# Kernel tuning notes

Measured on AMD Instinct MI355X. Metric: run time of the kernel, lower is better.

## Reference

```python
import jax, jax.numpy as jnp
import numpy as np

N, IN_DIM, H, K = 4096, 64, 64, 3
DT = 0.05


def graph_filter(z, S_powers, W):
    # z: [N, d_in], S_powers: [K, N, N], W: [K, d_in, d_out]
    zk = jnp.einsum('knm,md->knd', S_powers, z)   # K-hop diffused features
    return jnp.einsum('knd,kde->ne', zk, W)       # sum over taps k


def setup_inputs() -> dict:
    key = jax.random.key(0)
    ks = jax.random.split(key, 8)
    w_scale = 0.1
    return {
        'x': jax.random.normal(ks[0], (N, H), jnp.float32),
        'u': jax.random.normal(ks[1], (N, IN_DIM), jnp.float32),
        'S_powers': jax.random.normal(ks[2], (K, N, N), jnp.float32) / np.float32(np.sqrt(N)),
        'WA_hat': jax.random.normal(ks[3], (K, H, H), jnp.float32) * w_scale,
        'WB_hat': jax.random.normal(ks[4], (K, IN_DIM, H), jnp.float32) * w_scale,
        'WA_state': jax.random.normal(ks[5], (K, H, H), jnp.float32) * w_scale,
        'WB_state': jax.random.normal(ks[6], (K, IN_DIM, H), jnp.float32) * w_scale,
        'bx': jnp.zeros((1, H), jnp.float32),
        'bu': jnp.zeros((1, H), jnp.float32),
        'b': jnp.ones((1, H), jnp.float32) * 0.1,
        'n_steps': 4,
    }


def reference(x, u, S_powers, WA_hat, WB_hat, WA_state, WB_state, bx, bu, b, n_steps):
    # Input-driven terms are constant across solver steps; hoist them.
    fu = jax.nn.relu(graph_filter(u, S_powers, WB_hat) + bu)   # [N, H]
    sigma_c = jnp.tanh(graph_filter(u, S_powers, WB_state))    # [N, H]

    def step(xc, _):
        f = jax.nn.relu(graph_filter(xc, S_powers, WA_hat) + bx) + fu
        dx = -(b + f) * xc - graph_filter(xc, S_powers, WA_state) + f * sigma_c
        xn = jnp.clip(xc + DT * dx, -1.0, 1.0)
        return xn, None

    xf, _ = jax.lax.scan(step, x, None, length=n_steps)
    return xf
```

## Files before the change

### kernel.cpp

```cpp
#include <hip/hip_runtime.h>
#include <math.h>


typedef unsigned short u16;
typedef unsigned int u32;
typedef __attribute__((ext_vector_type(8))) short short8;
typedef __attribute__((ext_vector_type(4))) float f32x4;

#define NN 4096
#define HD 64
#define KB32 128
#define DT_C 0.05f

__device__ __forceinline__ u16 f2bf(float f) {
    u32 u = __float_as_uint(f);
    u += 0x7FFFu + ((u >> 16) & 1u);
    return (u16)(u >> 16);
}
__device__ __forceinline__ u32 pk2(float a, float b) {
    return (u32)f2bf(a) | ((u32)f2bf(b) << 16);
}

__global__ __launch_bounds__(256) void zprep_kernel(
    const float* __restrict__ u, const float* __restrict__ x,
    const float* __restrict__ WAh, const float* __restrict__ WAs,
    const float* __restrict__ WBh, const float* __restrict__ WBs,
    u16* __restrict__ utT, u16* __restrict__ xtT, u16* __restrict__ WtT)
{
    const int b = blockIdx.x;
    const int t = threadIdx.x;
    if (b < 256) {
        const float* z = (b < 128) ? u : x;
        u16* ztT = (b < 128) ? utT : xtT;
        const int kb = b & 127, n0 = kb * 32;
        __shared__ __align__(16) u16 tile[64][40];
        const int nl = t >> 3, c0 = (t & 7) * 8;
        const float* src = z + (size_t)(n0 + nl) * HD + c0;
        float4 f0 = ((const float4*)src)[0];
        float4 f1 = ((const float4*)src)[1];
        tile[c0 + 0][nl] = f2bf(f0.x); tile[c0 + 1][nl] = f2bf(f0.y);
        tile[c0 + 2][nl] = f2bf(f0.z); tile[c0 + 3][nl] = f2bf(f0.w);
        tile[c0 + 4][nl] = f2bf(f1.x); tile[c0 + 5][nl] = f2bf(f1.y);
        tile[c0 + 6][nl] = f2bf(f1.z); tile[c0 + 7][nl] = f2bf(f1.w);
        __syncthreads();
        const int e = t >> 2, kw0 = (t & 3) * 8;
        short8 v = *(const short8*)&tile[e][kw0];
        *(short8*)(ztT + ((size_t)kb * 64 + e) * 32 + kw0) = v;
    } else {
        for (int f = t; f < 4 * 6 * 64 * 32; f += 256) {
            int mat = f / 12288, r = f % 12288;
            int s = r / 2048, r2 = r % 2048;
            int e = r2 >> 5, kw = r2 & 31;
            int kp = s * 32 + kw, tap = kp >> 6, d = kp & 63;
            const float* Wm = (mat == 0) ? WAh : (mat == 1) ? WAs : (mat == 2) ? WBh : WBs;
            WtT[f] = f2bf(Wm[((size_t)tap * HD + d) * HD + e]);
        }
    }
}

__global__ __launch_bounds__(256) void diffuseA_kernel(
    const float* __restrict__ S, const u16* __restrict__ utT,
    const u16* __restrict__ xtT, u16* __restrict__ SbT,
    float* __restrict__ Yp, int iters)
{
    const int t = threadIdx.x;
    const int tap = blockIdx.z;
    const int row0 = blockIdx.x * 64;
    const int kb0 = blockIdx.y * iters;
    const int w = t >> 6, lane = t & 63, l15 = lane & 15, quad = lane >> 4;

    const int r0 = row0 + w * 16 + l15;
    const float* Sb = S + ((size_t)tap * NN + r0) * NN + quad * 8;
    u16* Wb = SbT + (((size_t)tap * KB32) * NN + r0) * 32 + quad * 8;

    f32x4 z4 = {0.f, 0.f, 0.f, 0.f};
    f32x4 acc[2][4];
    #pragma unroll
    for (int s = 0; s < 2; ++s)
        #pragma unroll
        for (int j = 0; j < 4; ++j) acc[s][j] = z4;

    #pragma unroll 4
    for (int it = 0; it < iters; ++it) {
        const int kb = kb0 + it;
        const float* sp0 = Sb + (size_t)kb * 32;
        float4 f0 = ((const float4*)sp0)[0];
        float4 f1 = ((const float4*)sp0)[1];
        union U { uint4 u4; short8 s8; };
        U A0;
        A0.u4.x = pk2(f0.x, f0.y); A0.u4.y = pk2(f0.z, f0.w);
        A0.u4.z = pk2(f1.x, f1.y); A0.u4.w = pk2(f1.z, f1.w);
        *(uint4*)(Wb + (size_t)kb * (NN * 32)) = A0.u4;
        #pragma unroll
        for (int ct = 0; ct < 4; ++ct) {
            const size_t bo = ((size_t)kb * 64 + ct * 16 + l15) * 32 + quad * 8;
            short8 bu = *(const short8*)(utT + bo);
            short8 bx = *(const short8*)(xtT + bo);
            acc[0][ct] = __builtin_amdgcn_mfma_f32_16x16x32_bf16(A0.s8, bu, acc[0][ct], 0, 0, 0);
            acc[1][ct] = __builtin_amdgcn_mfma_f32_16x16x32_bf16(A0.s8, bx, acc[1][ct], 0, 0, 0);
        }
    }
    #pragma unroll
    for (int s = 0; s < 2; ++s) {
        float* yb = Yp + ((size_t)((blockIdx.y * 3 + tap) * 2 + s) * NN + row0) * HD;
        #pragma unroll
        for (int ct = 0; ct < 4; ++ct)
            #pragma unroll
            for (int r = 0; r < 4; ++r)
                yb[(size_t)(w * 16 + quad * 4 + r) * HD + ct * 16 + l15] = acc[s][ct][r];
    }
}

__global__ __launch_bounds__(256) void diffuseS_kernel(
    const u16* __restrict__ SbT, const u16* __restrict__ xtT,
    float* __restrict__ Yp, int iters)
{
    const int t = threadIdx.x;
    const int tap = blockIdx.z;
    const int row0 = blockIdx.x * 64;
    const int kb0 = blockIdx.y * iters;
    const int w = t >> 6, lane = t & 63, l15 = lane & 15, quad = lane >> 4;

    const u16* A0 = SbT + (((size_t)(tap * KB32) * NN + row0 + w * 16 + l15) * 32) + quad * 8;
    const size_t arowstride = (size_t)NN * 32;

    f32x4 z4 = {0.f, 0.f, 0.f, 0.f};
    f32x4 acc[4];
    #pragma unroll
    for (int j = 0; j < 4; ++j) acc[j] = z4;

    #pragma unroll 4
    for (int it = 0; it < iters; ++it) {
        const int kb = kb0 + it;
        short8 a0 = *(const short8*)(A0 + (size_t)kb * arowstride);
        #pragma unroll
        for (int ct = 0; ct < 4; ++ct) {
            short8 bb = *(const short8*)(xtT + ((size_t)kb * 64 + ct * 16 + l15) * 32 + quad * 8);
            acc[ct] = __builtin_amdgcn_mfma_f32_16x16x32_bf16(a0, bb, acc[ct], 0, 0, 0);
        }
    }
    float* yb = Yp + ((size_t)(blockIdx.y * 3 + tap) * NN + row0) * HD;
    #pragma unroll
    for (int ct = 0; ct < 4; ++ct)
        #pragma unroll
        for (int r = 0; r < 4; ++r)
            yb[(size_t)(w * 16 + quad * 4 + r) * HD + ct * 16 + l15] = acc[ct][r];
}

__global__ __launch_bounds__(256) void update_step_kernel(
    const float* __restrict__ Yp, int KS, const u16* __restrict__ WtT,
    const float* __restrict__ bx, const float* __restrict__ bvec,
    const float* __restrict__ fu, const float* __restrict__ sc,
    const float* __restrict__ xc, float* __restrict__ xn,
    u16* __restrict__ xtT, int do_pack)
{
    __shared__ __align__(16) u16 yt[6][16][56];
    __shared__ __align__(16) u16 pkt[64][24];
    const int t = threadIdx.x;
    const int n0 = blockIdx.x * 16;

    for (int f = t; f < 384; f += 256) {
        const int tap = f >> 7;
        const int r = f & 127;
        const int nl = r >> 3, d8 = r & 7, d0 = d8 * 8;
        const float* p = Yp + ((size_t)tap * NN + n0 + nl) * HD + d0;
        const size_t kstride = (size_t)3 * NN * HD;
        float4 s0 = {0.f, 0.f, 0.f, 0.f}, s1 = {0.f, 0.f, 0.f, 0.f};
        for (int y = 0; y < KS; ++y) {
            float4 v0 = ((const float4*)(p + (size_t)y * kstride))[0];
            float4 v1 = ((const float4*)(p + (size_t)y * kstride))[1];
            s0.x += v0.x; s0.y += v0.y; s0.z += v0.z; s0.w += v0.w;
            s1.x += v1.x; s1.y += v1.y; s1.z += v1.z; s1.w += v1.w;
        }
        uint4 o;
        o.x = pk2(s0.x, s0.y); o.y = pk2(s0.z, s0.w);
        o.z = pk2(s1.x, s1.y); o.w = pk2(s1.z, s1.w);
        const int s = tap * 2 + (d8 >> 2), kw0 = (d8 & 3) * 8;
        *(uint4*)&yt[s][nl][kw0] = o;
    }
    __syncthreads();

    const int wv = t >> 6, lane = t & 63, l15 = lane & 15, quad = lane >> 4;
    f32x4 z4 = {0.f, 0.f, 0.f, 0.f};
    f32x4 aF = z4, aG = z4;
    #pragma unroll
    for (int s = 0; s < 6; ++s) {
        short8 a = *(const short8*)&yt[s][l15][quad * 8];
        const size_t wo = ((size_t)s * 64 + wv * 16 + l15) * 32 + quad * 8;
        short8 bF = *(const short8*)(WtT + wo);
        short8 bG = *(const short8*)(WtT + wo + 12288);
        aF = __builtin_amdgcn_mfma_f32_16x16x32_bf16(a, bF, aF, 0, 0, 0);
        aG = __builtin_amdgcn_mfma_f32_16x16x32_bf16(a, bG, aG, 0, 0, 0);
    }
    const int e = wv * 16 + l15;
    const float bxv = bx[e], bbv = bvec[e];
    float xos[4];
    #pragma unroll
    for (int r = 0; r < 4; ++r) {
        const int n = n0 + quad * 4 + r;
        const size_t o = (size_t)n * HD + e;
        float ff = fmaxf(aF[r] + bxv, 0.f) + fu[o];
        float xv = xc[o];
        float dx = -(bbv + ff) * xv - aG[r] + ff * sc[o];
        float xo = fminf(fmaxf(xv + DT_C * dx, -1.f), 1.f);
        xn[o] = xo;
        xos[r] = xo;
    }
    if (do_pack) {
        uint2 pv;
        pv.x = pk2(xos[0], xos[1]);
        pv.y = pk2(xos[2], xos[3]);
        *(uint2*)&pkt[e][quad * 4] = pv;
        __syncthreads();
        if (t < 128) {
            const int ee = t >> 1, g = t & 1;
            short8 v = *(const short8*)&pkt[ee][g * 8];
            const int kb = n0 >> 5;
            const int kwb = (n0 & 31) + g * 8;
            *(short8*)(xtT + ((size_t)kb * 64 + ee) * 32 + kwb) = v;
        }
    }
}

__global__ __launch_bounds__(256) void update1_kernel(
    const float* __restrict__ Yp, int KS, const u16* __restrict__ WtT,
    const float* __restrict__ bx, const float* __restrict__ bu,
    const float* __restrict__ bvec, const float* __restrict__ x0,
    float* __restrict__ fu, float* __restrict__ sc, float* __restrict__ x1,
    u16* __restrict__ xtT)
{
    __shared__ __align__(16) u16 yt[2][6][16][56];
    __shared__ __align__(16) u16 pkt[64][24];
    const int t = threadIdx.x;
    const int n0 = blockIdx.x * 16;

    #pragma unroll
    for (int ff = 0; ff < 3; ++ff) {
        const int f = t + ff * 256;
        const int src = f / 384;
        const int r3 = f - src * 384;
        const int tap = r3 >> 7;
        const int r = r3 & 127;
        const int nl = r >> 3, d8 = r & 7, d0 = d8 * 8;
        const float* p = Yp + (((size_t)(tap * 2 + src)) * NN + n0 + nl) * HD + d0;
        const size_t kstride = (size_t)6 * NN * HD;
        float4 s0 = {0.f, 0.f, 0.f, 0.f}, s1 = {0.f, 0.f, 0.f, 0.f};
        for (int y = 0; y < KS; ++y) {
            float4 v0 = ((const float4*)(p + (size_t)y * kstride))[0];
            float4 v1 = ((const float4*)(p + (size_t)y * kstride))[1];
            s0.x += v0.x; s0.y += v0.y; s0.z += v0.z; s0.w += v0.w;
            s1.x += v1.x; s1.y += v1.y; s1.z += v1.z; s1.w += v1.w;
        }
        uint4 o;
        o.x = pk2(s0.x, s0.y); o.y = pk2(s0.z, s0.w);
        o.z = pk2(s1.x, s1.y); o.w = pk2(s1.z, s1.w);
        const int s = tap * 2 + (d8 >> 2), kw0 = (d8 & 3) * 8;
        *(uint4*)&yt[src][s][nl][kw0] = o;
    }
    __syncthreads();

    const int wv = t >> 6, lane = t & 63, l15 = lane & 15, quad = lane >> 4;
    f32x4 z4 = {0.f, 0.f, 0.f, 0.f};
    f32x4 aF = z4, aG = z4, aFu = z4, aSc = z4;
    #pragma unroll
    for (int s = 0; s < 6; ++s) {
        short8 au = *(const short8*)&yt[0][s][l15][quad * 8];
        short8 ax = *(const short8*)&yt[1][s][l15][quad * 8];
        const size_t wo = ((size_t)s * 64 + wv * 16 + l15) * 32 + quad * 8;
        short8 bF  = *(const short8*)(WtT + wo);
        short8 bG  = *(const short8*)(WtT + wo + 12288);
        short8 bFu = *(const short8*)(WtT + wo + 2 * 12288);
        short8 bSc = *(const short8*)(WtT + wo + 3 * 12288);
        aF  = __builtin_amdgcn_mfma_f32_16x16x32_bf16(ax, bF,  aF,  0, 0, 0);
        aG  = __builtin_amdgcn_mfma_f32_16x16x32_bf16(ax, bG,  aG,  0, 0, 0);
        aFu = __builtin_amdgcn_mfma_f32_16x16x32_bf16(au, bFu, aFu, 0, 0, 0);
        aSc = __builtin_amdgcn_mfma_f32_16x16x32_bf16(au, bSc, aSc, 0, 0, 0);
    }
    const int e = wv * 16 + l15;
    const float bxv = bx[e], buv = bu[e], bbv = bvec[e];
    float xos[4];
    #pragma unroll
    for (int r = 0; r < 4; ++r) {
        const int n = n0 + quad * 4 + r;
        const size_t o = (size_t)n * HD + e;
        float fuv = fmaxf(aFu[r] + buv, 0.f);
        float scv = tanhf(aSc[r]);
        float ff = fmaxf(aF[r] + bxv, 0.f) + fuv;
        float xv = x0[o];
        float dx = -(bbv + ff) * xv - aG[r] + ff * scv;
        float xo = fminf(fmaxf(xv + DT_C * dx, -1.f), 1.f);
        fu[o] = fuv; sc[o] = scv; x1[o] = xo;
        xos[r] = xo;
    }
    {
        uint2 pv;
        pv.x = pk2(xos[0], xos[1]);
        pv.y = pk2(xos[2], xos[3]);
        *(uint2*)&pkt[e][quad * 4] = pv;
        __syncthreads();
        if (t < 128) {
            const int ee = t >> 1, g = t & 1;
            short8 v = *(const short8*)&pkt[ee][g * 8];
            const int kb = n0 >> 5;
            const int kwb = (n0 & 31) + g * 8;
            *(short8*)(xtT + ((size_t)kb * 64 + ee) * 32 + kwb) = v;
        }
    }
}

extern "C" void kernel_launch(void* const* d_in, const int* in_sizes, int n_in,
                              void* d_out, int out_size, void* d_ws, size_t ws_size,
                              hipStream_t stream) {
    const float* x   = (const float*)d_in[0];
    const float* u   = (const float*)d_in[1];
    const float* S   = (const float*)d_in[2];
    const float* WAh = (const float*)d_in[3];
    const float* WBh = (const float*)d_in[4];
    const float* WAs = (const float*)d_in[5];
    const float* WBs = (const float*)d_in[6];
    const float* bx  = (const float*)d_in[7];
    const float* bu  = (const float*)d_in[8];
    const float* bvec= (const float*)d_in[9];
    float* out = (float*)d_out;

    const size_t sbf_bytes = (size_t)3 * NN * NN * 2;
    const size_t slice = (size_t)NN * HD * 4;
    const size_t rest = 2 * 524288 + 98304 + 4 * 1048576;
    int KS_A = 8, KS_S = 8;
    if (ws_size < sbf_bytes + 48 * slice + rest) { KS_A = 4; KS_S = 8; }
    if (ws_size < sbf_bytes + 24 * slice + rest) { KS_A = 2; KS_S = 4; }
    if (ws_size < sbf_bytes + 12 * slice + rest) { KS_A = 1; KS_S = 2; }
    const int nslice = (KS_A * 6 > KS_S * 3) ? KS_A * 6 : KS_S * 3;

    char* p = (char*)d_ws;
    u16* SbT  = (u16*)p;         p += sbf_bytes;
    float* Yp = (float*)p;       p += (size_t)nslice * slice;
    u16* utT  = (u16*)p;         p += 524288;
    u16* xtT  = (u16*)p;         p += 524288;
    u16* WtT  = (u16*)p;         p += 98304;
    float* fu = (float*)p;       p += 1048576;
    float* sc = (float*)p;       p += 1048576;
    float* xA = (float*)p;       p += 1048576;
    float* xB = (float*)p;       p += 1048576;

    zprep_kernel<<<257, 256, 0, stream>>>(u, x, WAh, WAs, WBh, WBs, utT, xtT, WtT);

    diffuseA_kernel<<<dim3(64, KS_A, 3), 256, 0, stream>>>(S, utT, xtT, SbT, Yp, KB32 / KS_A);
    update1_kernel<<<256, 256, 0, stream>>>(Yp, KS_A, WtT, bx, bu, bvec, x, fu, sc, xA, xtT);

    diffuseS_kernel<<<dim3(64, KS_S, 3), 256, 0, stream>>>(SbT, xtT, Yp, KB32 / KS_S);
    update_step_kernel<<<256, 256, 0, stream>>>(Yp, KS_S, WtT, bx, bvec, fu, sc, xA, xB, xtT, 1);

    diffuseS_kernel<<<dim3(64, KS_S, 3), 256, 0, stream>>>(SbT, xtT, Yp, KB32 / KS_S);
    update_step_kernel<<<256, 256, 0, stream>>>(Yp, KS_S, WtT, bx, bvec, fu, sc, xB, xA, xtT, 1);

    diffuseS_kernel<<<dim3(64, KS_S, 3), 256, 0, stream>>>(SbT, xtT, Yp, KB32 / KS_S);
    update_step_kernel<<<256, 256, 0, stream>>>(Yp, KS_S, WtT, bx, bvec, fu, sc, xA, out, xtT, 0);
}
```

Before: 521.5 us.

## Fuse three taps per diffuseS block, swap MFMA operands for vector stores

diffuseS now handles all three taps in one block, so each loaded B fragment of xtT is reused across the three S taps instead of being reloaded per tap. The split-K factor for the step kernels rises from 8 to 16 to keep the grid filled after the tap dimension is removed. MFMA operand order is swapped in both diffuse kernels so each lane's accumulator holds contiguous output columns, allowing f32x4 vector stores in place of scalar strided stores. B loads in diffuseA are hoisted ahead of the conversion, and unroll drops from 4 to 2. The costs are more accumulator registers per thread and more partial-sum slices that the update kernel must reduce.

```diff
diff --git a/kernel.cpp b/kernel.cpp
--- a/kernel.cpp
+++ b/kernel.cpp
@@ -69,9 +69,9 @@
     const int kb0 = blockIdx.y * iters;
     const int w = t >> 6, lane = t & 63, l15 = lane & 15, quad = lane >> 4;
 
-    const int r0 = row0 + w * 16 + l15;
-    const float* Sb = S + ((size_t)tap * NN + r0) * NN + quad * 8;
-    u16* Wb = SbT + (((size_t)tap * KB32) * NN + r0) * 32 + quad * 8;
+    const int n = row0 + w * 16 + l15;
+    const float* Sb = S + ((size_t)tap * NN + n) * NN + quad * 8;
+    u16* Wb = SbT + (((size_t)tap * KB32) * NN + n) * 32 + quad * 8;
 
     f32x4 z4 = {0.f, 0.f, 0.f, 0.f};
     f32x4 acc[2][4];
@@ -80,12 +80,19 @@
         #pragma unroll
         for (int j = 0; j < 4; ++j) acc[s][j] = z4;
 
-    #pragma unroll 4
+    #pragma unroll 2
     for (int it = 0; it < iters; ++it) {
         const int kb = kb0 + it;
         const float* sp0 = Sb + (size_t)kb * 32;
         float4 f0 = ((const float4*)sp0)[0];
         float4 f1 = ((const float4*)sp0)[1];
+        short8 bu[4], bx[4];
+        #pragma unroll
+        for (int ct = 0; ct < 4; ++ct) {
+            const size_t bo = ((size_t)kb * 64 + ct * 16 + l15) * 32 + quad * 8;
+            bu[ct] = *(const short8*)(utT + bo);
+            bx[ct] = *(const short8*)(xtT + bo);
+        }
         union U { uint4 u4; short8 s8; };
         U A0;
         A0.u4.x = pk2(f0.x, f0.y); A0.u4.y = pk2(f0.z, f0.w);
@@ -93,21 +100,16 @@
         *(uint4*)(Wb + (size_t)kb * (NN * 32)) = A0.u4;
         #pragma unroll
         for (int ct = 0; ct < 4; ++ct) {
-            const size_t bo = ((size_t)kb * 64 + ct * 16 + l15) * 32 + quad * 8;
-            short8 bu = *(const short8*)(utT + bo);
-            short8 bx = *(const short8*)(xtT + bo);
-            acc[0][ct] = __builtin_amdgcn_mfma_f32_16x16x32_bf16(A0.s8, bu, acc[0][ct], 0, 0, 0);
-            acc[1][ct] = __builtin_amdgcn_mfma_f32_16x16x32_bf16(A0.s8, bx, acc[1][ct], 0, 0, 0);
+            acc[0][ct] = __builtin_amdgcn_mfma_f32_16x16x32_bf16(bu[ct], A0.s8, acc[0][ct], 0, 0, 0);
+            acc[1][ct] = __builtin_amdgcn_mfma_f32_16x16x32_bf16(bx[ct], A0.s8, acc[1][ct], 0, 0, 0);
         }
     }
     #pragma unroll
     for (int s = 0; s < 2; ++s) {
-        float* yb = Yp + ((size_t)((blockIdx.y * 3 + tap) * 2 + s) * NN + row0) * HD;
+        float* yb = Yp + ((size_t)((blockIdx.y * 3 + tap) * 2 + s) * NN + n) * HD + quad * 4;
         #pragma unroll
         for (int ct = 0; ct < 4; ++ct)
-            #pragma unroll
-            for (int r = 0; r < 4; ++r)
-                yb[(size_t)(w * 16 + quad * 4 + r) * HD + ct * 16 + l15] = acc[s][ct][r];
+            *(f32x4*)(yb + ct * 16) = acc[s][ct];
     }
 }
 
@@ -116,35 +118,46 @@
     float* __restrict__ Yp, int iters)
 {
     const int t = threadIdx.x;
-    const int tap = blockIdx.z;
     const int row0 = blockIdx.x * 64;
     const int kb0 = blockIdx.y * iters;
     const int w = t >> 6, lane = t & 63, l15 = lane & 15, quad = lane >> 4;
 
-    const u16* A0 = SbT + (((size_t)(tap * KB32) * NN + row0 + w * 16 + l15) * 32) + quad * 8;
-    const size_t arowstride = (size_t)NN * 32;
+    const int n = row0 + w * 16 + l15;
+    const u16* A0 = SbT + (size_t)n * 32 + quad * 8;
+    const size_t kstr = (size_t)NN * 32;
+    const size_t tstr = (size_t)KB32 * NN * 32;
 
     f32x4 z4 = {0.f, 0.f, 0.f, 0.f};
-    f32x4 acc[4];
-    #pragma unroll
-    for (int j = 0; j < 4; ++j) acc[j] = z4;
-
-    #pragma unroll 4
+    f32x4 acc[3][4];
+    #pragma unroll
+    for (int tp = 0; tp < 3; ++tp)
+        #pragma unroll
+        for (int j = 0; j < 4; ++j) acc[tp][j] = z4;
+
+    #pragma unroll 2
     for (int it = 0; it < iters; ++it) {
         const int kb = kb0 + it;
-        short8 a0 = *(const short8*)(A0 + (size_t)kb * arowstride);
-        #pragma unroll
-        for (int ct = 0; ct < 4; ++ct) {
-            short8 bb = *(const short8*)(xtT + ((size_t)kb * 64 + ct * 16 + l15) * 32 + quad * 8);
-            acc[ct] = __builtin_amdgcn_mfma_f32_16x16x32_bf16(a0, bb, acc[ct], 0, 0, 0);
-        }
-    }
-    float* yb = Yp + ((size_t)(blockIdx.y * 3 + tap) * NN + row0) * HD;
-    #pragma unroll
-    for (int ct = 0; ct < 4; ++ct)
-        #pragma unroll
-        for (int r = 0; r < 4; ++r)
-            yb[(size_t)(w * 16 + quad * 4 + r) * HD + ct * 16 + l15] = acc[ct][r];
+        short8 a[3];
+        #pragma unroll
+        for (int tp = 0; tp < 3; ++tp)
+            a[tp] = *(const short8*)(A0 + (size_t)tp * tstr + (size_t)kb * kstr);
+        short8 b[4];
+        #pragma unroll
+        for (int ct = 0; ct < 4; ++ct)
+            b[ct] = *(const short8*)(xtT + ((size_t)kb * 64 + ct * 16 + l15) * 32 + quad * 8);
+        #pragma unroll
+        for (int tp = 0; tp < 3; ++tp)
+            #pragma unroll
+            for (int ct = 0; ct < 4; ++ct)
+                acc[tp][ct] = __builtin_amdgcn_mfma_f32_16x16x32_bf16(b[ct], a[tp], acc[tp][ct], 0, 0, 0);
+    }
+    #pragma unroll
+    for (int tp = 0; tp < 3; ++tp) {
+        float* yb = Yp + ((size_t)(blockIdx.y * 3 + tp) * NN + n) * HD + quad * 4;
+        #pragma unroll
+        for (int ct = 0; ct < 4; ++ct)
+            *(f32x4*)(yb + ct * 16) = acc[tp][ct];
+    }
 }
 
 __global__ __launch_bounds__(256) void update_step_kernel(
@@ -326,7 +339,7 @@
     const size_t sbf_bytes = (size_t)3 * NN * NN * 2;
     const size_t slice = (size_t)NN * HD * 4;
     const size_t rest = 2 * 524288 + 98304 + 4 * 1048576;
-    int KS_A = 8, KS_S = 8;
+    int KS_A = 8, KS_S = 16;
     if (ws_size < sbf_bytes + 48 * slice + rest) { KS_A = 4; KS_S = 8; }
     if (ws_size < sbf_bytes + 24 * slice + rest) { KS_A = 2; KS_S = 4; }
     if (ws_size < sbf_bytes + 12 * slice + rest) { KS_A = 1; KS_S = 2; }
@@ -348,12 +361,12 @@
     diffuseA_kernel<<<dim3(64, KS_A, 3), 256, 0, stream>>>(S, utT, xtT, SbT, Yp, KB32 / KS_A);
     update1_kernel<<<256, 256, 0, stream>>>(Yp, KS_A, WtT, bx, bu, bvec, x, fu, sc, xA, xtT);
 
-    diffuseS_kernel<<<dim3(64, KS_S, 3), 256, 0, stream>>>(SbT, xtT, Yp, KB32 / KS_S);
+    diffuseS_kernel<<<dim3(64, KS_S), 256, 0, stream>>>(SbT, xtT, Yp, KB32 / KS_S);
     update_step_kernel<<<256, 256, 0, stream>>>(Yp, KS_S, WtT, bx, bvec, fu, sc, xA, xB, xtT, 1);
 
-    diffuseS_kernel<<<dim3(64, KS_S, 3), 256, 0, stream>>>(SbT, xtT, Yp, KB32 / KS_S);
+    diffuseS_kernel<<<dim3(64, KS_S), 256, 0, stream>>>(SbT, xtT, Yp, KB32 / KS_S);
     update_step_kernel<<<256, 256, 0, stream>>>(Yp, KS_S, WtT, bx, bvec, fu, sc, xB, xA, xtT, 1);
 
-    diffuseS_kernel<<<dim3(64, KS_S, 3), 256, 0, stream>>>(SbT, xtT, Yp, KB32 / KS_S);
+    diffuseS_kernel<<<dim3(64, KS_S), 256, 0, stream>>>(SbT, xtT, Yp, KB32 / KS_S);
     update_step_kernel<<<256, 256, 0, stream>>>(Yp, KS_S, WtT, bx, bvec, fu, sc, xA, out, xtT, 0);
 }
```

Result: no change. 520.8 us (-0.1%).
